# Kernel optimization log

Hardware: AMD Instinct MI355X
Metric: run time of the kernel (lower is better)

Reference implementation:

```python
import jax, jax.numpy as jnp
import numpy as np

EMB = 1024
HEAD = 64
B = 4
S = 4096


def setup_inputs() -> dict:
    key = jax.random.key(0)
    ks = jax.random.split(key, 7)
    std = 1.0 / np.sqrt(EMB)
    return {
        "x": jax.random.normal(ks[0], (B, S, EMB), dtype=jnp.float32),
        "Wq": jax.random.uniform(ks[1], (EMB, HEAD), jnp.float32, -std, std),
        "bq": jax.random.uniform(ks[2], (HEAD,), jnp.float32, -std, std),
        "Wk": jax.random.uniform(ks[3], (EMB, HEAD), jnp.float32, -std, std),
        "bk": jax.random.uniform(ks[4], (HEAD,), jnp.float32, -std, std),
        "Wv": jax.random.uniform(ks[5], (EMB, HEAD), jnp.float32, -std, std),
        "bv": jax.random.uniform(ks[6], (HEAD,), jnp.float32, -std, std),
    }


def reference(x, Wq, bq, Wk, bk, Wv, bv):
    # Q, K, V: [B, S, HEAD]
    Q = x @ Wq + bq
    K = x @ Wk + bk
    V = x @ Wv + bv
    scale = 1.0 / jnp.sqrt(jnp.asarray(HEAD, dtype=Q.dtype))
    # scores: [B, S, S]
    scores = jnp.einsum("bqd,bkd->bqk", Q, K) * scale
    seq = x.shape[1]
    # original mask = tril(randn) sliced; masked_fill where mask==0 => causal
    causal = jnp.tril(jnp.ones((seq, seq), dtype=bool))
    scores = jnp.where(causal, scores, -jnp.inf)
    attn = jax.nn.softmax(scores, axis=-1)
    return jnp.einsum("bqk,bkd->bqd", attn, V)
```

## Files before the change

kernel.cpp:

```cpp
#include <hip/hip_runtime.h>
#include <stdint.h>

#define S_LEN 4096
#define EMB   1024
#define HEAD  64

typedef short bf16x8 __attribute__((ext_vector_type(8)));
typedef float f32x4  __attribute__((ext_vector_type(4)));

#define QSCALE 0.18033688011112042f

__device__ __forceinline__ unsigned short f2bf(float f) {
    union { float f; uint32_t u; } v; v.f = f;
    uint32_t r = v.u + 0x7fffu + ((v.u >> 16) & 1u);
    return (unsigned short)(r >> 16);
}

__global__ void wprep_kernel(const float* __restrict__ Wq,
                             const float* __restrict__ Wk,
                             const float* __restrict__ Wv,
                             unsigned short* __restrict__ wt) {
    __shared__ float t[64][65];
    const int tid = threadIdx.x;
    const int m   = blockIdx.x >> 4;
    const int k0  = (blockIdx.x & 15) << 6;
    const float* W = (m == 0) ? Wq : (m == 1) ? Wk : Wv;
    for (int i = 0; i < 4; ++i) {
        const int k  = (tid >> 4) + i * 16;
        const int n4 = (tid & 15) << 2;
        float4 v = *(const float4*)&W[(k0 + k) * 64 + n4];
        t[k][n4 + 0] = v.x; t[k][n4 + 1] = v.y;
        t[k][n4 + 2] = v.z; t[k][n4 + 3] = v.w;
    }
    __syncthreads();
    const int n = tid >> 2, kq = (tid & 3) << 4;
    __align__(16) unsigned short u[16];
    for (int i = 0; i < 16; ++i) u[i] = f2bf(t[kq + i][n]);
    *(int4*)&wt[(m * 64 + n) * 1024 + k0 + kq]     = *(int4*)&u[0];
    *(int4*)&wt[(m * 64 + n) * 1024 + k0 + kq + 8] = *(int4*)&u[8];
}

__global__ __launch_bounds__(512, 2) void qkv_kernel(
    const float* __restrict__ x, const unsigned short* __restrict__ wt,
    const float* __restrict__ bq, const float* __restrict__ bk,
    const float* __restrict__ bv,
    unsigned short* __restrict__ Qp, unsigned short* __restrict__ Kp,
    unsigned short* __restrict__ Vt) {

    __shared__ __align__(16) unsigned short xs[2][32 * 72];
    __shared__ __align__(16) unsigned short ws[2][192 * 72];

    const int tid  = threadIdx.x;
    const int lane = tid & 63;
    const int w    = tid >> 6;
    const int wm   = w & 1;
    const int wn   = w >> 1;
    const int quad = lane >> 4;
    const int lid  = lane & 15;
    const int row0 = blockIdx.x * 32;

    f32x4 acc[3];
    for (int j = 0; j < 3; ++j) acc[j] = (f32x4){0.f, 0.f, 0.f, 0.f};

#define STAGE(BUF, K0)                                                         \
    do {                                                                       \
        {           \
            int r = tid >> 4, c4 = (tid & 15) << 2;                            \
            float4 v = *(const float4*)&x[(row0 + r) * EMB + (K0) + c4];       \
            ushort4 u;                                                         \
            u.x = f2bf(v.x); u.y = f2bf(v.y); u.z = f2bf(v.z); u.w = f2bf(v.w);\
            *(ushort4*)&xs[BUF][r * 72 + c4] = u;                              \
        }                                                                      \
        for (int i = 0; i < 3; ++i) {      \
            int f = tid + i * 512;                                             \
            int n = f >> 3, kq = (f & 7) << 3;                                 \
            *(int4*)&ws[BUF][n * 72 + kq] =                                    \
                *(const int4*)&wt[(n << 10) + (K0) + kq];                      \
        }                                                                      \
    } while (0)

    STAGE(0, 0);
    __syncthreads();

    for (int kc = 0; kc < 16; ++kc) {
        const int cur = kc & 1;
        if (kc + 1 < 16) STAGE(cur ^ 1, (kc + 1) * 64);
        for (int kk = 0; kk < 2; ++kk) {
            bf16x8 a = *(const bf16x8*)&xs[cur][(wm * 16 + lid) * 72 + kk * 32 + quad * 8];
            for (int nt = 0; nt < 3; ++nt) {
                bf16x8 bfr = *(const bf16x8*)&ws[cur][(wn * 48 + nt * 16 + lid) * 72 + kk * 32 + quad * 8];
                acc[nt] = __builtin_amdgcn_mfma_f32_16x16x32_bf16(a, bfr, acc[nt], 0, 0, 0);
            }
        }
        __syncthreads();
    }
#undef STAGE

    for (int nt = 0; nt < 3; ++nt) {
        const int col = wn * 48 + nt * 16 + lid;
        const int mid = col >> 6;
        const int lc  = col & 63;
        const float bias = (mid == 0) ? bq[lc] : (mid == 1) ? bk[lc] : bv[lc];
        const int rb = row0 + wm * 16 + quad * 4;
        f32x4 v = acc[nt];
        if (mid == 0) {
            for (int j = 0; j < 4; ++j)
                Qp[(rb + j) * 64 + lc] = f2bf((v[j] + bias) * QSCALE);
        } else if (mid == 1) {
            for (int j = 0; j < 4; ++j)
                Kp[(rb + j) * 64 + lc] = f2bf(v[j] + bias);
        } else {
            const int bb = rb >> 12, s = rb & 4095;
            ushort4 u;
            u.x = f2bf(v[0] + bias); u.y = f2bf(v[1] + bias);
            u.z = f2bf(v[2] + bias); u.w = f2bf(v[3] + bias);
            *(ushort4*)&Vt[(bb * 64 + lc) * S_LEN + s] = u;
        }
    }
}

__global__ __launch_bounds__(512, 2) void flash_kernel(
    const unsigned short* __restrict__ Qp, const unsigned short* __restrict__ Kp,
    const unsigned short* __restrict__ Vt, float* __restrict__ out) {

    __shared__ __align__(16) union {
        unsigned short Ps[8][2][16 * 72];
        struct { float Obuf[8][32][66]; float lbuf[8][32]; } c;
    } sh;

    const int tid  = threadIdx.x;
    const int lane = tid & 63;
    const int w    = tid >> 6;
    const int quad = lane >> 4;
    const int lid  = lane & 15;

    const int l  = blockIdx.x;
    const int x  = l & 7;
    const int m  = l >> 3;
    const int j  = m & 31;
    const int r  = m >> 5;
    const int b  = x & 3;
    const int h  = x >> 2;
    const int qt = (h == 0) ? (r ? j : 127 - j)
                            : (r ? 32 + j : 95 - j);
    const int q0 = qt * 32;
    const int nt = (q0 >> 6) + 1;

    bf16x8 qf[2][2];
    for (int mt = 0; mt < 2; ++mt) {
        const int qrow = b * S_LEN + q0 + mt * 16 + lid;
        qf[mt][0] = *(const bf16x8*)&Qp[qrow * 64 + quad * 8];
        qf[mt][1] = *(const bf16x8*)&Qp[qrow * 64 + 32 + quad * 8];
    }

    const f32x4 zero = {0.f, 0.f, 0.f, 0.f};
    f32x4 O[2][4];
    for (int mt = 0; mt < 2; ++mt)
        for (int dt = 0; dt < 4; ++dt) O[mt][dt] = zero;
    float ls[2][4] = {{0.f, 0.f, 0.f, 0.f}, {0.f, 0.f, 0.f, 0.f}};

    const unsigned short* Kb = &Kp[b * S_LEN * 64];
    const unsigned short* Vb = &Vt[b * 64 * S_LEN];

    int t = w;
    bf16x8 kf[4][2];
    if (t < nt) {
        const int kt = t << 6;
        for (int sub = 0; sub < 4; ++sub) {
            const int krow = (kt + sub * 16 + lid) * 64;
            kf[sub][0] = *(const bf16x8*)&Kb[krow + quad * 8];
            kf[sub][1] = *(const bf16x8*)&Kb[krow + 32 + quad * 8];
        }
    }

    while (t < nt) {
        const int kt = t << 6;
        bf16x8 vf[4][2];
        for (int sub = 0; sub < 4; ++sub) {
            const int vrow = (sub * 16 + lid) * S_LEN + kt;
            vf[sub][0] = *(const bf16x8*)&Vb[vrow + quad * 8];
            vf[sub][1] = *(const bf16x8*)&Vb[vrow + 32 + quad * 8];
        }
        f32x4 S0[4], S1[4];
        for (int sub = 0; sub < 4; ++sub) {
            S0[sub] = __builtin_amdgcn_mfma_f32_16x16x32_bf16(qf[0][0], kf[sub][0], zero, 0, 0, 0);
            S0[sub] = __builtin_amdgcn_mfma_f32_16x16x32_bf16(qf[0][1], kf[sub][1], S0[sub], 0, 0, 0);
            S1[sub] = __builtin_amdgcn_mfma_f32_16x16x32_bf16(qf[1][0], kf[sub][0], zero, 0, 0, 0);
            S1[sub] = __builtin_amdgcn_mfma_f32_16x16x32_bf16(qf[1][1], kf[sub][1], S1[sub], 0, 0, 0);
        }
        const int tn = t + 8;
        if (tn < nt) {
            const int ktn = tn << 6;
            for (int sub = 0; sub < 4; ++sub) {
                const int krow = (ktn + sub * 16 + lid) * 64;
                kf[sub][0] = *(const bf16x8*)&Kb[krow + quad * 8];
                kf[sub][1] = *(const bf16x8*)&Kb[krow + 32 + quad * 8];
            }
        }
        if (t == nt - 1) {
            for (int sub = 0; sub < 4; ++sub) {
                const int kc = kt + sub * 16 + lid;
                for (int jj = 0; jj < 4; ++jj) {
                    if (kc > q0 + quad * 4 + jj)      S0[sub][jj] = -1e30f;
                    if (kc > q0 + 16 + quad * 4 + jj) S1[sub][jj] = -1e30f;
                }
            }
        }
        unsigned short* ps0 = &sh.Ps[w][0][0];
        unsigned short* ps1 = &sh.Ps[w][1][0];
        for (int sub = 0; sub < 4; ++sub)
            for (int jj = 0; jj < 4; ++jj) {
                const float p0 = exp2f(S0[sub][jj]);
                const float p1 = exp2f(S1[sub][jj]);
                ls[0][jj] += p0;
                ls[1][jj] += p1;
                ps0[(quad * 4 + jj) * 72 + sub * 16 + lid] = f2bf(p0);
                ps1[(quad * 4 + jj) * 72 + sub * 16 + lid] = f2bf(p1);
            }
        asm volatile("s_waitcnt lgkmcnt(0)" ::: "memory");
        bf16x8 pf[2][2];
        pf[0][0] = *(const bf16x8*)&ps0[lid * 72 + quad * 8];
        pf[0][1] = *(const bf16x8*)&ps0[lid * 72 + 32 + quad * 8];
        pf[1][0] = *(const bf16x8*)&ps1[lid * 72 + quad * 8];
        pf[1][1] = *(const bf16x8*)&ps1[lid * 72 + 32 + quad * 8];
        for (int dt = 0; dt < 4; ++dt)
            for (int mt = 0; mt < 2; ++mt) {
                O[mt][dt] = __builtin_amdgcn_mfma_f32_16x16x32_bf16(pf[mt][0], vf[dt][0], O[mt][dt], 0, 0, 0);
                O[mt][dt] = __builtin_amdgcn_mfma_f32_16x16x32_bf16(pf[mt][1], vf[dt][1], O[mt][dt], 0, 0, 0);
            }
        t = tn;
    }

    __syncthreads();

    for (int mt = 0; mt < 2; ++mt)
        for (int jj = 0; jj < 4; ++jj) {
            float rs = ls[mt][jj];
            for (int off = 1; off < 16; off <<= 1) rs += __shfl_xor(rs, off, 64);
            const int row = mt * 16 + quad * 4 + jj;
            if (lid == 0) sh.c.lbuf[w][row] = rs;
            for (int dt = 0; dt < 4; ++dt)
                sh.c.Obuf[w][row][dt * 16 + lid] = O[mt][dt][jj];
        }
    __syncthreads();

    const int col = tid & 63;
    const int r0  = tid >> 6;
    for (int ii = 0; ii < 4; ++ii) {
        const int row = r0 + ii * 8;
        float o = 0.f, lsum = 0.f;
        for (int ww = 0; ww < 8; ++ww) {
            o    += sh.c.Obuf[ww][row][col];
            lsum += sh.c.lbuf[ww][row];
        }
        out[(b * S_LEN + q0 + row) * 64 + col] = o / lsum;
    }
}

extern "C" void kernel_launch(void* const* d_in, const int* in_sizes, int n_in,
                              void* d_out, int out_size, void* d_ws, size_t ws_size,
                              hipStream_t stream) {
    const float* x  = (const float*)d_in[0];
    const float* Wq = (const float*)d_in[1];
    const float* bq = (const float*)d_in[2];
    const float* Wk = (const float*)d_in[3];
    const float* bk = (const float*)d_in[4];
    const float* Wv = (const float*)d_in[5];
    const float* bv = (const float*)d_in[6];
    float* out = (float*)d_out;

    unsigned short* wt = (unsigned short*)d_ws;
    unsigned short* Qp = wt + 196608;
    unsigned short* Kp = Qp + 1048576;
    unsigned short* Vt = Kp + 1048576;

    hipLaunchKernelGGL(wprep_kernel, dim3(48), dim3(256), 0, stream, Wq, Wk, Wv, wt);
    hipLaunchKernelGGL(qkv_kernel, dim3(512), dim3(512), 0, stream,
                       x, wt, bq, bk, bv, Qp, Kp, Vt);
    hipLaunchKernelGGL(flash_kernel, dim3(512), dim3(512), 0, stream,
                       Qp, Kp, Vt, out);
}
```

Measured before the change: 165.4 us.

## Use 32x32 MFMA with transposed scores and register-only P via permlane32 swap

Restructures the flash attention inner loop to use 32x32x16 bf16 MFMA. It computes S^T = K·Q^T so each lane holds one query row's probabilities, then repacks them into the A-operand layout with v_cvt_pk_bf16 and permlane32_swap instead of a round trip through LDS. Key tiles shrink from 64 to 32 keys per wave iteration, and s_setprio is added around the MFMA blocks. This removes the per-iteration LDS stores, the wait, and the LDS reloads of P, at the cost of twice as many loop iterations and more dependence on the exact MFMA register layout.

Result: faster. 154.7 us (-6.5%).

```diff
diff --git a/kernel.cpp b/kernel.cpp
--- a/kernel.cpp
+++ b/kernel.cpp
@@ -7,6 +7,7 @@
 
 typedef short bf16x8 __attribute__((ext_vector_type(8)));
 typedef float f32x4  __attribute__((ext_vector_type(4)));
+typedef float f32x16 __attribute__((ext_vector_type(16)));
 
 #define QSCALE 0.18033688011112042f
 
@@ -14,6 +15,12 @@
     union { float f; uint32_t u; } v; v.f = f;
     uint32_t r = v.u + 0x7fffu + ((v.u >> 16) & 1u);
     return (unsigned short)(r >> 16);
+}
+
+__device__ __forceinline__ int cvtpk_bf16(float lo, float hi_) {
+    int r;
+    asm("v_cvt_pk_bf16_f32 %0, %1, %2" : "=v"(r) : "v"(lo), "v"(hi_));
+    return r;
 }
 
 __global__ void wprep_kernel(const float* __restrict__ Wq,
@@ -123,16 +130,14 @@
     const unsigned short* __restrict__ Qp, const unsigned short* __restrict__ Kp,
     const unsigned short* __restrict__ Vt, float* __restrict__ out) {
 
-    __shared__ __align__(16) union {
-        unsigned short Ps[8][2][16 * 72];
-        struct { float Obuf[8][32][66]; float lbuf[8][32]; } c;
-    } sh;
+    __shared__ __align__(16) float Obuf[8][32][66];
+    __shared__ float lbuf[8][32];
 
     const int tid  = threadIdx.x;
     const int lane = tid & 63;
     const int w    = tid >> 6;
-    const int quad = lane >> 4;
-    const int lid  = lane & 15;
+    const int hi   = lane >> 5;
+    const int l5   = lane & 31;
 
     const int l  = blockIdx.x;
     const int x  = l & 7;
@@ -144,104 +149,91 @@
     const int qt = (h == 0) ? (r ? j : 127 - j)
                             : (r ? 32 + j : 95 - j);
     const int q0 = qt * 32;
-    const int nt = (q0 >> 6) + 1;
-
-    bf16x8 qf[2][2];
-    for (int mt = 0; mt < 2; ++mt) {
-        const int qrow = b * S_LEN + q0 + mt * 16 + lid;
-        qf[mt][0] = *(const bf16x8*)&Qp[qrow * 64 + quad * 8];
-        qf[mt][1] = *(const bf16x8*)&Qp[qrow * 64 + 32 + quad * 8];
-    }
-
-    const f32x4 zero = {0.f, 0.f, 0.f, 0.f};
-    f32x4 O[2][4];
-    for (int mt = 0; mt < 2; ++mt)
-        for (int dt = 0; dt < 4; ++dt) O[mt][dt] = zero;
-    float ls[2][4] = {{0.f, 0.f, 0.f, 0.f}, {0.f, 0.f, 0.f, 0.f}};
+    const int nt = qt + 1;
+
+    bf16x8 qf[4];
+#pragma unroll
+    for (int dk = 0; dk < 4; ++dk)
+        qf[dk] = *(const bf16x8*)&Qp[(b * S_LEN + q0 + l5) * 64 + dk * 16 + hi * 8];
+
+    f32x16 O0 = {}, O1 = {};
+    float ls = 0.f;
 
     const unsigned short* Kb = &Kp[b * S_LEN * 64];
     const unsigned short* Vb = &Vt[b * 64 * S_LEN];
 
     int t = w;
-    bf16x8 kf[4][2];
+    bf16x8 kf[4];
     if (t < nt) {
-        const int kt = t << 6;
-        for (int sub = 0; sub < 4; ++sub) {
-            const int krow = (kt + sub * 16 + lid) * 64;
-            kf[sub][0] = *(const bf16x8*)&Kb[krow + quad * 8];
-            kf[sub][1] = *(const bf16x8*)&Kb[krow + 32 + quad * 8];
-        }
+#pragma unroll
+        for (int dk = 0; dk < 4; ++dk)
+            kf[dk] = *(const bf16x8*)&Kb[(t * 32 + l5) * 64 + dk * 16 + hi * 8];
     }
 
     while (t < nt) {
-        const int kt = t << 6;
-        bf16x8 vf[4][2];
-        for (int sub = 0; sub < 4; ++sub) {
-            const int vrow = (sub * 16 + lid) * S_LEN + kt;
-            vf[sub][0] = *(const bf16x8*)&Vb[vrow + quad * 8];
-            vf[sub][1] = *(const bf16x8*)&Vb[vrow + 32 + quad * 8];
-        }
-        f32x4 S0[4], S1[4];
-        for (int sub = 0; sub < 4; ++sub) {
-            S0[sub] = __builtin_amdgcn_mfma_f32_16x16x32_bf16(qf[0][0], kf[sub][0], zero, 0, 0, 0);
-            S0[sub] = __builtin_amdgcn_mfma_f32_16x16x32_bf16(qf[0][1], kf[sub][1], S0[sub], 0, 0, 0);
-            S1[sub] = __builtin_amdgcn_mfma_f32_16x16x32_bf16(qf[1][0], kf[sub][0], zero, 0, 0, 0);
-            S1[sub] = __builtin_amdgcn_mfma_f32_16x16x32_bf16(qf[1][1], kf[sub][1], S1[sub], 0, 0, 0);
-        }
+        const int kt = t << 5;
+        bf16x8 vf[2][2];
+#pragma unroll
+        for (int dh = 0; dh < 2; ++dh)
+#pragma unroll
+            for (int kc = 0; kc < 2; ++kc)
+                vf[dh][kc] = *(const bf16x8*)&Vb[(dh * 32 + l5) * S_LEN + kt + kc * 16 + hi * 8];
+
+        __builtin_amdgcn_s_setprio(1);
+        f32x16 st = {};
+#pragma unroll
+        for (int dk = 0; dk < 4; ++dk)
+            st = __builtin_amdgcn_mfma_f32_32x32x16_bf16(kf[dk], qf[dk], st, 0, 0, 0);
+        __builtin_amdgcn_s_setprio(0);
+
         const int tn = t + 8;
         if (tn < nt) {
-            const int ktn = tn << 6;
-            for (int sub = 0; sub < 4; ++sub) {
-                const int krow = (ktn + sub * 16 + lid) * 64;
-                kf[sub][0] = *(const bf16x8*)&Kb[krow + quad * 8];
-                kf[sub][1] = *(const bf16x8*)&Kb[krow + 32 + quad * 8];
+#pragma unroll
+            for (int dk = 0; dk < 4; ++dk)
+                kf[dk] = *(const bf16x8*)&Kb[(tn * 32 + l5) * 64 + dk * 16 + hi * 8];
+        }
+
+        if (t == nt - 1) {
+#pragma unroll
+            for (int rr = 0; rr < 16; ++rr) {
+                const int key = kt + (rr & 3) + 8 * (rr >> 2) + 4 * hi;
+                if (key > q0 + l5) st[rr] = -1e30f;
             }
         }
-        if (t == nt - 1) {
-            for (int sub = 0; sub < 4; ++sub) {
-                const int kc = kt + sub * 16 + lid;
-                for (int jj = 0; jj < 4; ++jj) {
-                    if (kc > q0 + quad * 4 + jj)      S0[sub][jj] = -1e30f;
-                    if (kc > q0 + 16 + quad * 4 + jj) S1[sub][jj] = -1e30f;
-                }
-            }
-        }
-        unsigned short* ps0 = &sh.Ps[w][0][0];
-        unsigned short* ps1 = &sh.Ps[w][1][0];
-        for (int sub = 0; sub < 4; ++sub)
-            for (int jj = 0; jj < 4; ++jj) {
-                const float p0 = exp2f(S0[sub][jj]);
-                const float p1 = exp2f(S1[sub][jj]);
-                ls[0][jj] += p0;
-                ls[1][jj] += p1;
-                ps0[(quad * 4 + jj) * 72 + sub * 16 + lid] = f2bf(p0);
-                ps1[(quad * 4 + jj) * 72 + sub * 16 + lid] = f2bf(p1);
-            }
-        asm volatile("s_waitcnt lgkmcnt(0)" ::: "memory");
-        bf16x8 pf[2][2];
-        pf[0][0] = *(const bf16x8*)&ps0[lid * 72 + quad * 8];
-        pf[0][1] = *(const bf16x8*)&ps0[lid * 72 + 32 + quad * 8];
-        pf[1][0] = *(const bf16x8*)&ps1[lid * 72 + quad * 8];
-        pf[1][1] = *(const bf16x8*)&ps1[lid * 72 + 32 + quad * 8];
-        for (int dt = 0; dt < 4; ++dt)
-            for (int mt = 0; mt < 2; ++mt) {
-                O[mt][dt] = __builtin_amdgcn_mfma_f32_16x16x32_bf16(pf[mt][0], vf[dt][0], O[mt][dt], 0, 0, 0);
-                O[mt][dt] = __builtin_amdgcn_mfma_f32_16x16x32_bf16(pf[mt][1], vf[dt][1], O[mt][dt], 0, 0, 0);
-            }
+
+#pragma unroll
+        for (int kc = 0; kc < 2; ++kc) {
+            const int c8 = kc * 8;
+            float ev[8];
+#pragma unroll
+            for (int i = 0; i < 8; ++i) ev[i] = exp2f(st[c8 + i]);
+            ls += ((ev[0] + ev[1]) + (ev[2] + ev[3])) +
+                  ((ev[4] + ev[5]) + (ev[6] + ev[7]));
+            const int p0 = cvtpk_bf16(ev[0], ev[1]);
+            const int p1 = cvtpk_bf16(ev[2], ev[3]);
+            const int p2 = cvtpk_bf16(ev[4], ev[5]);
+            const int p3 = cvtpk_bf16(ev[6], ev[7]);
+            auto s02 = __builtin_amdgcn_permlane32_swap(p0, p2, false, false);
+            auto s13 = __builtin_amdgcn_permlane32_swap(p1, p3, false, false);
+            union { int wd[4]; bf16x8 v; } pf;
+            pf.wd[0] = s02[0]; pf.wd[1] = s13[0];
+            pf.wd[2] = s02[1]; pf.wd[3] = s13[1];
+            __builtin_amdgcn_s_setprio(1);
+            O0 = __builtin_amdgcn_mfma_f32_32x32x16_bf16(pf.v, vf[0][kc], O0, 0, 0, 0);
+            O1 = __builtin_amdgcn_mfma_f32_32x32x16_bf16(pf.v, vf[1][kc], O1, 0, 0, 0);
+            __builtin_amdgcn_s_setprio(0);
+        }
         t = tn;
     }
 
-    __syncthreads();
-
-    for (int mt = 0; mt < 2; ++mt)
-        for (int jj = 0; jj < 4; ++jj) {
-            float rs = ls[mt][jj];
-            for (int off = 1; off < 16; off <<= 1) rs += __shfl_xor(rs, off, 64);
-            const int row = mt * 16 + quad * 4 + jj;
-            if (lid == 0) sh.c.lbuf[w][row] = rs;
-            for (int dt = 0; dt < 4; ++dt)
-                sh.c.Obuf[w][row][dt * 16 + lid] = O[mt][dt][jj];
-        }
+    const float lt = ls + __shfl_xor(ls, 32);
+#pragma unroll
+    for (int rr = 0; rr < 16; ++rr) {
+        const int row = (rr & 3) + 8 * (rr >> 2) + 4 * hi;
+        Obuf[w][row][l5]      = O0[rr];
+        Obuf[w][row][32 + l5] = O1[rr];
+    }
+    if (lane < 32) lbuf[w][l5] = lt;
     __syncthreads();
 
     const int col = tid & 63;
@@ -250,8 +242,8 @@
         const int row = r0 + ii * 8;
         float o = 0.f, lsum = 0.f;
         for (int ww = 0; ww < 8; ++ww) {
-            o    += sh.c.Obuf[ww][row][col];
-            lsum += sh.c.lbuf[ww][row];
+            o    += Obuf[ww][row][col];
+            lsum += lbuf[ww][row];
         }
         out[(b * S_LEN + q0 + row) * 64 + col] = o / lsum;
     }
```
